# Kernel tuning notes

Hardware: AMD Instinct MI355X
Metric: run time of the kernel (lower is better)

The kernel has to match this reference:

```python
import jax, jax.numpy as jnp
import numpy as np

N, E, HID, H = 20000, 200000, 96, 6
HC = H * HID  # 576


def _ln(x, g, b):
    mu = x.mean(-1, keepdims=True)
    v = ((x - mu) ** 2).mean(-1, keepdims=True)
    return (x - mu) / jnp.sqrt(v + 1e-5) * g + b


def _gatv2(x, edge_emb, src, dst, Wl, bl, Wr, br, We, attw, cbias):
    # PyG GATv2Conv, concat=False, edge_dim=HID, eval mode (no dropout)
    xl = (x @ Wl + bl).reshape(N, H, HID)   # source transform (lin_l)
    xr = (x @ Wr + br).reshape(N, H, HID)   # target transform (lin_r)
    ee = (edge_emb @ We).reshape(E, H, HID) # lin_edge (no bias in PyG)
    h = jax.nn.leaky_relu(xl[src] + xr[dst] + ee, 0.2)   # [E,H,C]
    logits = jnp.einsum('ehc,hc->eh', h, attw)            # [E,H]
    m = jax.ops.segment_max(logits, dst, num_segments=N)  # segment softmax over dst
    ex = jnp.exp(logits - m[dst])
    den = jax.ops.segment_sum(ex, dst, num_segments=N)
    alpha = ex / (den[dst] + 1e-16)
    out = jax.ops.segment_sum(xl[src] * alpha[..., None], dst, num_segments=N)  # [N,H,C]
    return out.mean(axis=1) + cbias  # concat=False -> head mean, then bias


def _forward(x, edge_attr, ne_w, ne_b, ne_g, ne_beta, ee_w, ee_b, ee_g, ee_beta,
             Wl, bl, Wr, br, We, attw, cbias, lng, lnb,
             p1_w, p1_b, p1_g, p1_beta, p2_w, p2_b, p2_g, p2_beta, p3_w, p3_b,
             edge_index):
    src, dst = edge_index[0], edge_index[1]
    x = jax.nn.relu(_ln(x @ ne_w + ne_b, ne_g, ne_beta))
    edge_emb = jax.nn.relu(_ln(edge_attr @ ee_w + ee_b, ee_g, ee_beta))
    for i in range(3):  # fixed small layer count
        h = _gatv2(x, edge_emb, src, dst, Wl[i], bl[i], Wr[i], br[i], We[i], attw[i], cbias[i])
        if i < 2:
            h = jax.nn.elu(h)
        x = x + _ln(h, lng[i], lnb[i])
    ctx = jnp.concatenate([x[src], x[dst], edge_emb], axis=1)  # [E, 3*HID]
    h = jax.nn.relu(_ln(ctx @ p1_w + p1_b, p1_g, p1_beta))
    h = jax.nn.relu(_ln(h @ p2_w + p2_b, p2_g, p2_beta))
    return h @ p3_w + p3_b  # [E,1]


def setup_inputs():
    key = jax.random.key(0)
    ks = jax.random.split(key, 16)
    g = lambda k, shape, s: jax.random.normal(k, shape, dtype=jnp.float32) * s
    inp = {}
    inp['x'] = g(ks[0], (N, 4), 1.0)
    inp['edge_attr'] = g(ks[1], (E, 3), 1.0)
    inp['edge_index'] = jax.random.randint(ks[2], (2, E), 0, N, dtype=jnp.int32)
    # encoders
    inp['ne_w'] = g(ks[3], (4, HID), 0.5); inp['ne_b'] = jnp.zeros((HID,), jnp.float32)
    inp['ne_g'] = jnp.ones((HID,), jnp.float32); inp['ne_beta'] = jnp.zeros((HID,), jnp.float32)
    inp['ee_w'] = g(ks[4], (3, HID), 0.5); inp['ee_b'] = jnp.zeros((HID,), jnp.float32)
    inp['ee_g'] = jnp.ones((HID,), jnp.float32); inp['ee_beta'] = jnp.zeros((HID,), jnp.float32)
    # 3 stacked GATv2 layers
    inp['Wl'] = g(ks[5], (3, HID, HC), 0.1); inp['bl'] = jnp.zeros((3, HC), jnp.float32)
    inp['Wr'] = g(ks[6], (3, HID, HC), 0.1); inp['br'] = jnp.zeros((3, HC), jnp.float32)
    inp['We'] = g(ks[7], (3, HID, HC), 0.1)
    inp['attw'] = g(ks[8], (3, H, HID), 0.1)
    inp['cbias'] = jnp.zeros((3, HID), jnp.float32)
    inp['lng'] = jnp.ones((3, HID), jnp.float32); inp['lnb'] = jnp.zeros((3, HID), jnp.float32)
    # predictor MLP
    inp['p1_w'] = g(ks[9], (3 * HID, 128), 0.1); inp['p1_b'] = jnp.zeros((128,), jnp.float32)
    inp['p1_g'] = jnp.ones((128,), jnp.float32); inp['p1_beta'] = jnp.zeros((128,), jnp.float32)
    inp['p2_w'] = g(ks[10], (128, 64), 0.1); inp['p2_b'] = jnp.zeros((64,), jnp.float32)
    inp['p2_g'] = jnp.ones((64,), jnp.float32); inp['p2_beta'] = jnp.zeros((64,), jnp.float32)
    inp['p3_w'] = g(ks[11], (64, 1), 0.1); inp['p3_b'] = jnp.zeros((1,), jnp.float32)
    return inp


def reference(x, edge_attr, edge_index, ne_w, ne_b, ne_g, ne_beta, ee_w, ee_b, ee_g, ee_beta,
              Wl, bl, Wr, br, We, attw, cbias, lng, lnb,
              p1_w, p1_b, p1_g, p1_beta, p2_w, p2_b, p2_g, p2_beta, p3_w, p3_b):
    return _forward(x, edge_attr, ne_w, ne_b, ne_g, ne_beta, ee_w, ee_b, ee_g, ee_beta,
                    Wl, bl, Wr, br, We, attw, cbias, lng, lnb,
                    p1_w, p1_b, p1_g, p1_beta, p2_w, p2_b, p2_g, p2_beta, p3_w, p3_b,
                    edge_index)
```

## Files before the change

### kernel.cpp

```cpp
#include <hip/hip_runtime.h>
#include <math.h>

#define NN 20000
#define NE 200000

typedef __attribute__((ext_vector_type(8))) short bf16x8;
typedef __attribute__((ext_vector_type(8))) unsigned short u16x8;
typedef __attribute__((ext_vector_type(4))) float f32x4;

__device__ __forceinline__ unsigned short f2bf(float x) {
  union { float f; unsigned u; } c; c.f = x;
  unsigned r = c.u + 0x7FFF + ((c.u >> 16) & 1);
  return (unsigned short)(r >> 16);
}
__device__ __forceinline__ float bf2f(unsigned short u) {
  union { unsigned u; float f; } c; c.u = ((unsigned)u) << 16;
  return c.f;
}

template <int D>
__global__ __launch_bounds__(256) void encode_row_kernel(
    const float* __restrict__ in,
    const float* __restrict__ W, const float* __restrict__ b,
    const float* __restrict__ g, const float* __restrict__ beta,
    float* __restrict__ out, unsigned short* __restrict__ outb, int R) {
  int row = blockIdx.x * 256 + threadIdx.x;
  if (row >= R) return;
  float vin[D];
#pragma unroll
  for (int k = 0; k < D; k++) vin[k] = in[(size_t)row * D + k];
  float y[96];
  float s = 0.f, s2 = 0.f;
#pragma unroll
  for (int j = 0; j < 96; j++) {
    float v = b[j];
#pragma unroll
    for (int k = 0; k < D; k++) v += vin[k] * W[k * 96 + j];
    y[j] = v;
    s += v;
    s2 += v * v;
  }
  float mu = s * (1.f / 96.f);
  float var = s2 * (1.f / 96.f) - mu * mu;
  float rs = rsqrtf(var + 1e-5f);
#pragma unroll
  for (int c = 0; c < 12; c++) {
    u16x8 pk;
    float yo[8];
#pragma unroll
    for (int j = 0; j < 8; j++) {
      int jj = c * 8 + j;
      float v = (y[jj] - mu) * rs * g[jj] + beta[jj];
      v = fmaxf(v, 0.f);
      yo[j] = v;
      pk[j] = f2bf(v);
    }
    *(u16x8*)&outb[(size_t)row * 96 + c * 8] = pk;
    if (out) {
      f32x4 o0 = {yo[0], yo[1], yo[2], yo[3]};
      f32x4 o1 = {yo[4], yo[5], yo[6], yo[7]};
      *(f32x4*)&out[(size_t)row * 96 + c * 8] = o0;
      *(f32x4*)&out[(size_t)row * 96 + c * 8 + 4] = o1;
    }
  }
}

__global__ void convW_kernel(const float* __restrict__ We,
                             unsigned short* __restrict__ WeTb,
                             const float* __restrict__ Wl,
                             unsigned short* __restrict__ WlTb,
                             const float* __restrict__ Wr,
                             unsigned short* __restrict__ WrTb,
                             const float* __restrict__ p1w,
                             unsigned short* __restrict__ p1wT,
                             const float* __restrict__ p2w,
                             unsigned short* __restrict__ p2wT) {
  int idx = blockIdx.x * 256 + threadIdx.x;
  if (idx < 3 * 576 * 96) {
    int l = idx / (576 * 96);
    int rem = idx % (576 * 96);
    int n = rem / 96, k = rem % 96;
    size_t sidx = (size_t)l * 96 * 576 + (size_t)k * 576 + n;
    WeTb[idx] = f2bf(We[sidx]);
    WlTb[idx] = f2bf(Wl[sidx]);
    WrTb[idx] = f2bf(Wr[sidx]);
  }
  if (idx < 128 * 288) {
    int n = idx / 288, k = idx % 288;
    p1wT[idx] = f2bf(p1w[(size_t)k * 128 + n]);
  }
  if (idx < 64 * 128) {
    int n = idx / 128, k = idx % 128;
    p2wT[idx] = f2bf(p2w[(size_t)k * 64 + n]);
  }
}

__global__ void hist_kernel(const int* __restrict__ dst, int* __restrict__ deg) {
  int e = blockIdx.x * blockDim.x + threadIdx.x;
  if (e < NE) atomicAdd(&deg[dst[e]], 1);
}

__global__ __launch_bounds__(1024) void scan_kernel(
    const int* __restrict__ deg, int* __restrict__ rowptr, int* __restrict__ cursor) {
  __shared__ int wsum[16];
  int t = threadIdx.x;
  int base = t * 20;
  int loc[20];
  int s = 0;
#pragma unroll
  for (int j = 0; j < 20; j++) {
    int idx = base + j;
    int v = (idx < NN) ? deg[idx] : 0;
    loc[j] = s;
    s += v;
  }
  int lane = t & 63, wv = t >> 6;
  int inc = s;
#pragma unroll
  for (int off = 1; off < 64; off <<= 1) {
    int up = __shfl_up(inc, off);
    if (lane >= off) inc += up;
  }
  if (lane == 63) wsum[wv] = inc;
  __syncthreads();
  if (wv == 0) {
    int wval = (lane < 16) ? wsum[lane] : 0;
#pragma unroll
    for (int off = 1; off < 16; off <<= 1) {
      int up = __shfl_up(wval, off);
      if (lane >= off) wval += up;
    }
    if (lane < 16) wsum[lane] = wval;
  }
  __syncthreads();
  int wbase = (wv > 0) ? wsum[wv - 1] : 0;
  int excl = wbase + inc - s;
#pragma unroll
  for (int j = 0; j < 20; j++) {
    int idx = base + j;
    if (idx < NN) { rowptr[idx] = excl + loc[j]; cursor[idx] = excl + loc[j]; }
  }
  if (t == 0) rowptr[NN] = NE;
}

__global__ void scatter_kernel(const int* __restrict__ src,
                               const int* __restrict__ dst,
                               int* __restrict__ cursor, int* __restrict__ eidx,
                               int* __restrict__ srcp, int* __restrict__ dstp) {
  int e = blockIdx.x * blockDim.x + threadIdx.x;
  if (e < NE) {
    int d = dst[e];
    int p = atomicAdd(&cursor[d], 1);
    eidx[p] = e;
    srcp[p] = src[e];
    dstp[p] = d;
  }
}

__global__ __launch_bounds__(256) void xlxr_mfma_kernel(
    const unsigned short* __restrict__ Xb,
    const unsigned short* __restrict__ WlTb,
    const float* __restrict__ bl,
    const unsigned short* __restrict__ WrTb,
    const float* __restrict__ br,
    unsigned short* __restrict__ xlb, unsigned short* __restrict__ xrb) {
  int t = threadIdx.x;
  int wave = t >> 6, lane = t & 63;
  int l15 = lane & 15, quad = lane >> 4;
  int node = blockIdx.x * 64 + wave * 16 + l15;
  int nclamp = (node < NN) ? node : (NN - 1);
  bool valid = node < NN;
  const unsigned short* brow = &Xb[(size_t)nclamp * 96 + quad * 8];
  bf16x8 b0 = *(const bf16x8*)&brow[0];
  bf16x8 b1 = *(const bf16x8*)&brow[32];
  bf16x8 b2 = *(const bf16x8*)&brow[64];
#pragma unroll
  for (int mt = 0; mt < 36; mt++) {
    int wc = mt * 16 + l15;
    const unsigned short* aL = &WlTb[(size_t)wc * 96 + quad * 8];
    f32x4 accL = {0.f, 0.f, 0.f, 0.f};
    accL = __builtin_amdgcn_mfma_f32_16x16x32_bf16(*(const bf16x8*)&aL[0], b0, accL, 0, 0, 0);
    accL = __builtin_amdgcn_mfma_f32_16x16x32_bf16(*(const bf16x8*)&aL[32], b1, accL, 0, 0, 0);
    accL = __builtin_amdgcn_mfma_f32_16x16x32_bf16(*(const bf16x8*)&aL[64], b2, accL, 0, 0, 0);
    const unsigned short* aR = &WrTb[(size_t)wc * 96 + quad * 8];
    f32x4 accR = {0.f, 0.f, 0.f, 0.f};
    accR = __builtin_amdgcn_mfma_f32_16x16x32_bf16(*(const bf16x8*)&aR[0], b0, accR, 0, 0, 0);
    accR = __builtin_amdgcn_mfma_f32_16x16x32_bf16(*(const bf16x8*)&aR[32], b1, accR, 0, 0, 0);
    accR = __builtin_amdgcn_mfma_f32_16x16x32_bf16(*(const bf16x8*)&aR[64], b2, accR, 0, 0, 0);
    if (valid) {
      int c0 = mt * 16 + quad * 4;
      float4 bbL = *(const float4*)&bl[c0];
      float4 bbR = *(const float4*)&br[c0];
      ushort4 pL, pR;
      pL.x = f2bf(accL[0] + bbL.x); pL.y = f2bf(accL[1] + bbL.y);
      pL.z = f2bf(accL[2] + bbL.z); pL.w = f2bf(accL[3] + bbL.w);
      pR.x = f2bf(accR[0] + bbR.x); pR.y = f2bf(accR[1] + bbR.y);
      pR.z = f2bf(accR[2] + bbR.z); pR.w = f2bf(accR[3] + bbR.w);
      *(ushort4*)&xlb[(size_t)node * 576 + c0] = pL;
      *(ushort4*)&xrb[(size_t)node * 576 + c0] = pR;
    }
  }
}

__global__ __launch_bounds__(256) void logits_mfma_kernel(
    const unsigned short* __restrict__ EMBb,
    const unsigned short* __restrict__ WeTb,
    const float* __restrict__ attw,
    const unsigned short* __restrict__ XLb,
    const unsigned short* __restrict__ XRb,
    const int* __restrict__ eidx, const int* __restrict__ srcp,
    const int* __restrict__ dstp,
    float* __restrict__ logp) {
  __shared__ __align__(16) unsigned short emb[64][104];
  __shared__ __align__(16) unsigned short eeb[64][200];
  __shared__ int sd[64][2];
  int t = threadIdx.x;
  int p0 = blockIdx.x * 64;
  if (t < 128) sd[t >> 1][t & 1] = (t & 1) ? dstp[p0 + (t >> 1)] : srcp[p0 + (t >> 1)];
  {
    int e = t >> 2, c0 = (t & 3) * 24;
    int erow = eidx[p0 + e];
    const unsigned short* sp = &EMBb[(size_t)erow * 96 + c0];
    *(bf16x8*)&emb[e][c0]      = *(const bf16x8*)&sp[0];
    *(bf16x8*)&emb[e][c0 + 8]  = *(const bf16x8*)&sp[8];
    *(bf16x8*)&emb[e][c0 + 16] = *(const bf16x8*)&sp[16];
  }
  __syncthreads();

  int wave = t >> 6, lane = t & 63;
  int l15 = lane & 15, quad = lane >> 4;
  int el = t >> 2;
  int cq = (t & 3) * 24;
  int gsrc = sd[el][0];
  int gdst = sd[el][1];

  for (int hp = 0; hp < 3; hp++) {
    int h0 = hp * 2, h1 = hp * 2 + 1;
    const unsigned short* xl0 = &XLb[(size_t)gsrc * 576 + h0 * 96 + cq];
    const unsigned short* xr0 = &XRb[(size_t)gdst * 576 + h0 * 96 + cq];
    const unsigned short* xl1 = &XLb[(size_t)gsrc * 576 + h1 * 96 + cq];
    const unsigned short* xr1 = &XRb[(size_t)gdst * 576 + h1 * 96 + cq];
    bf16x8 gl0[3], gr0[3], gl1[3], gr1[3];
#pragma unroll
    for (int c8 = 0; c8 < 3; c8++) {
      gl0[c8] = *(const bf16x8*)&xl0[c8 * 8];
      gr0[c8] = *(const bf16x8*)&xr0[c8 * 8];
      gl1[c8] = *(const bf16x8*)&xl1[c8 * 8];
      gr1[c8] = *(const bf16x8*)&xr1[c8 * 8];
    }
#pragma unroll
    for (int k = 0; k < 3; k++) {
      int ntg = wave * 3 + k;
      int col = hp * 192 + ntg * 16 + l15;
      const unsigned short* brow = &WeTb[(size_t)col * 96 + quad * 8];
      bf16x8 b0 = *(const bf16x8*)&brow[0];
      bf16x8 b1 = *(const bf16x8*)&brow[32];
      bf16x8 b2 = *(const bf16x8*)&brow[64];
#pragma unroll
      for (int et = 0; et < 4; et++) {
        const unsigned short* ar = &emb[et * 16 + l15][quad * 8];
        bf16x8 a0 = *(const bf16x8*)&ar[0];
        bf16x8 a1 = *(const bf16x8*)&ar[32];
        bf16x8 a2 = *(const bf16x8*)&ar[64];
        f32x4 acc = {0.f, 0.f, 0.f, 0.f};
        acc = __builtin_amdgcn_mfma_f32_16x16x32_bf16(a0, b0, acc, 0, 0, 0);
        acc = __builtin_amdgcn_mfma_f32_16x16x32_bf16(a1, b1, acc, 0, 0, 0);
        acc = __builtin_amdgcn_mfma_f32_16x16x32_bf16(a2, b2, acc, 0, 0, 0);
#pragma unroll
        for (int r = 0; r < 4; r++)
          eeb[et * 16 + quad * 4 + r][ntg * 16 + l15] = f2bf(acc[r]);
      }
    }
    __syncthreads();
    float pl0 = 0.f, pl1 = 0.f;
    {
      const unsigned short* ee0 = &eeb[el][cq];
      const unsigned short* ee1 = &eeb[el][96 + cq];
      const f32x4* ap0 = (const f32x4*)&attw[h0 * 96 + cq];
      const f32x4* ap1 = (const f32x4*)&attw[h1 * 96 + cq];
#pragma unroll
      for (int c8 = 0; c8 < 3; c8++) {
        bf16x8 ev0 = *(const bf16x8*)&ee0[c8 * 8];
        bf16x8 ev1 = *(const bf16x8*)&ee1[c8 * 8];
        f32x4 a00 = ap0[c8 * 2], a01 = ap0[c8 * 2 + 1];
        f32x4 a10 = ap1[c8 * 2], a11 = ap1[c8 * 2 + 1];
#pragma unroll
        for (int j = 0; j < 4; j++) {
          float v0 = bf2f((unsigned short)ev0[j]) +
                     bf2f((unsigned short)gl0[c8][j]) +
                     bf2f((unsigned short)gr0[c8][j]);
          v0 = (v0 > 0.f) ? v0 : 0.2f * v0;
          pl0 += v0 * a00[j];
          float w0 = bf2f((unsigned short)ev0[j + 4]) +
                     bf2f((unsigned short)gl0[c8][j + 4]) +
                     bf2f((unsigned short)gr0[c8][j + 4]);
          w0 = (w0 > 0.f) ? w0 : 0.2f * w0;
          pl0 += w0 * a01[j];
          float v1 = bf2f((unsigned short)ev1[j]) +
                     bf2f((unsigned short)gl1[c8][j]) +
                     bf2f((unsigned short)gr1[c8][j]);
          v1 = (v1 > 0.f) ? v1 : 0.2f * v1;
          pl1 += v1 * a10[j];
          float w1 = bf2f((unsigned short)ev1[j + 4]) +
                     bf2f((unsigned short)gl1[c8][j + 4]) +
                     bf2f((unsigned short)gr1[c8][j + 4]);
          w1 = (w1 > 0.f) ? w1 : 0.2f * w1;
          pl1 += w1 * a11[j];
        }
      }
    }
    pl0 += __shfl_xor(pl0, 1); pl0 += __shfl_xor(pl0, 2);
    pl1 += __shfl_xor(pl1, 1); pl1 += __shfl_xor(pl1, 2);
    if ((t & 3) == 0) {
      size_t base = (size_t)(p0 + el) * 6 + hp * 2;
      logp[base] = pl0;
      logp[base + 1] = pl1;
    }
    __syncthreads();
  }
}

__global__ __launch_bounds__(256) void alpha_kernel(
    const float* __restrict__ logp, const int* __restrict__ rowptr,
    float* __restrict__ alpha) {
  int node = blockIdx.x * 4 + (threadIdx.x >> 6);
  int lane = threadIdx.x & 63;
  if (node >= NN) return;
  int r0 = rowptr[node], r1 = rowptr[node + 1];
  int d = r1 - r0;
  if (d == 0) return;
  if (d <= 64) {
    bool act = lane < d;
    int p = r0 + (act ? lane : (d - 1));
    float lg[6];
#pragma unroll
    for (int h = 0; h < 6; h++) lg[h] = logp[(size_t)p * 6 + h];
#pragma unroll
    for (int h = 0; h < 6; h++) {
      float m = act ? lg[h] : -1e30f;
#pragma unroll
      for (int off = 32; off > 0; off >>= 1) m = fmaxf(m, __shfl_xor(m, off));
      float w = act ? expf(lg[h] - m) : 0.f;
      float s = w;
#pragma unroll
      for (int off = 32; off > 0; off >>= 1) s += __shfl_xor(s, off);
      if (act) alpha[(size_t)p * 6 + h] = w / (s + 1e-16f);
    }
  } else {
    float m[6], s[6];
#pragma unroll
    for (int h = 0; h < 6; h++) { m[h] = -1e30f; s[h] = 0.f; }
    for (int cs = 0; cs < d; cs += 64) {
      int cnt = min(64, d - cs);
      bool act = lane < cnt;
      int p = r0 + cs + (act ? lane : (cnt - 1));
#pragma unroll
      for (int h = 0; h < 6; h++) {
        float lg = act ? logp[(size_t)p * 6 + h] : -1e30f;
        float cm = lg;
#pragma unroll
        for (int off = 32; off > 0; off >>= 1) cm = fmaxf(cm, __shfl_xor(cm, off));
        float newm = fmaxf(m[h], cm);
        float w = act ? expf(lg - newm) : 0.f;
        float ss = w;
#pragma unroll
        for (int off = 32; off > 0; off >>= 1) ss += __shfl_xor(ss, off);
        s[h] = s[h] * expf(m[h] - newm) + ss;
        m[h] = newm;
      }
    }
    float inv[6];
#pragma unroll
    for (int h = 0; h < 6; h++) inv[h] = 1.f / (s[h] + 1e-16f);
    for (int cs = 0; cs < d; cs += 64) {
      int cnt = min(64, d - cs);
      if (lane < cnt) {
        int p = r0 + cs + lane;
#pragma unroll
        for (int h = 0; h < 6; h++)
          alpha[(size_t)p * 6 + h] =
              expf(logp[(size_t)p * 6 + h] - m[h]) * inv[h];
      }
    }
  }
}

__global__ __launch_bounds__(576) void aggregate_kernel(
    float* __restrict__ x, unsigned short* __restrict__ xb,
    const unsigned short* __restrict__ XLb,
    const float* __restrict__ alpha, const int* __restrict__ rowptr,
    const int* __restrict__ srcp,
    const float* __restrict__ cbias, const float* __restrict__ lng,
    const float* __restrict__ lnb, int do_elu) {
  int t = threadIdx.x;
  int nb = t / 96, c = t % 96;
  int n = blockIdx.x * 6 + nb;
  bool vn = (n < NN);
  __shared__ float fin[6][96];
  __shared__ float red[6][2];
  int wave = t >> 6, lane = t & 63;
  int r0 = 0, d = 0;
  if (vn) { r0 = rowptr[n]; d = rowptr[n + 1] - r0; }
  float acc = 0.f;
  int j = 0;
  for (; j + 1 < d; j += 2) {
    int p = r0 + j;
    int s0 = srcp[p], s1 = srcp[p + 1];
    const float* ap0 = &alpha[(size_t)p * 6];
    float2 a00 = *(const float2*)&ap0[0];
    float2 a01 = *(const float2*)&ap0[2];
    float2 a02 = *(const float2*)&ap0[4];
    float2 a10 = *(const float2*)&ap0[6];
    float2 a11 = *(const float2*)&ap0[8];
    float2 a12 = *(const float2*)&ap0[10];
    const unsigned short* xp0 = &XLb[(size_t)s0 * 576 + c];
    const unsigned short* xp1 = &XLb[(size_t)s1 * 576 + c];
    unsigned short v00 = xp0[0],   v01 = xp0[96],  v02 = xp0[192];
    unsigned short v03 = xp0[288], v04 = xp0[384], v05 = xp0[480];
    unsigned short v10 = xp1[0],   v11 = xp1[96],  v12 = xp1[192];
    unsigned short v13 = xp1[288], v14 = xp1[384], v15 = xp1[480];
    acc += a00.x * bf2f(v00) + a00.y * bf2f(v01) + a01.x * bf2f(v02) +
           a01.y * bf2f(v03) + a02.x * bf2f(v04) + a02.y * bf2f(v05);
    acc += a10.x * bf2f(v10) + a10.y * bf2f(v11) + a11.x * bf2f(v12) +
           a11.y * bf2f(v13) + a12.x * bf2f(v14) + a12.y * bf2f(v15);
  }
  if (j < d) {
    int p = r0 + j;
    int s0 = srcp[p];
    const float* ap0 = &alpha[(size_t)p * 6];
    float2 a00 = *(const float2*)&ap0[0];
    float2 a01 = *(const float2*)&ap0[2];
    float2 a02 = *(const float2*)&ap0[4];
    const unsigned short* xp0 = &XLb[(size_t)s0 * 576 + c];
    unsigned short v00 = xp0[0],   v01 = xp0[96],  v02 = xp0[192];
    unsigned short v03 = xp0[288], v04 = xp0[384], v05 = xp0[480];
    acc += a00.x * bf2f(v00) + a00.y * bf2f(v01) + a01.x * bf2f(v02) +
           a01.y * bf2f(v03) + a02.x * bf2f(v04) + a02.y * bf2f(v05);
  }
  float fv = 0.f;
  if (vn) {
    float s = acc * (1.f / 6.f) + cbias[c];
    if (do_elu) s = (s > 0.f) ? s : expm1f(s);
    fv = s;
  }
  fin[nb][c] = fv;
  __syncthreads();
  if (wave < 6) {
    float x0 = fin[wave][lane];
    float x1 = (lane < 32) ? fin[wave][64 + lane] : 0.f;
    float s = x0 + x1;
    float s2 = x0 * x0 + x1 * x1;
#pragma unroll
    for (int off = 32; off > 0; off >>= 1) {
      s += __shfl_xor(s, off);
      s2 += __shfl_xor(s2, off);
    }
    if (lane == 0) {
      float mu = s * (1.f / 96.f);
      float var = s2 * (1.f / 96.f) - mu * mu;
      red[wave][0] = mu;
      red[wave][1] = rsqrtf(var + 1e-5f);
    }
  }
  __syncthreads();
  if (vn) {
    float y = (fv - red[nb][0]) * red[nb][1] * lng[c] + lnb[c];
    float nv = x[(size_t)n * 96 + c] + y;
    x[(size_t)n * 96 + c] = nv;
    xb[(size_t)n * 96 + c] = f2bf(nv);
  }
}

__global__ __launch_bounds__(256) void pred_mfma_kernel(
    const unsigned short* __restrict__ Xb,
    const unsigned short* __restrict__ EMBb,
    const int* __restrict__ src, const int* __restrict__ dst,
    const unsigned short* __restrict__ p1wT,
    const float* __restrict__ p1b, const float* __restrict__ p1g,
    const float* __restrict__ p1be,
    const unsigned short* __restrict__ p2wT,
    const float* __restrict__ p2b, const float* __restrict__ p2g,
    const float* __restrict__ p2be,
    const float* __restrict__ p3w, const float* __restrict__ p3b,
    float* __restrict__ out) {
  __shared__ __align__(16) unsigned short fragB[4 * 9 * 64 * 8];
  __shared__ unsigned short h1s[4][16][136];
  int t = threadIdx.x;
  int wave = t >> 6, lane = t & 63;
  int l15 = lane & 15, quad = lane >> 4;
  int ebase = blockIdx.x * 64 + wave * 16;
  int erow = ebase + l15;
  int sN = src[erow], dN = dst[erow];

  bf16x8 A[9];
  const unsigned short* xs = &Xb[(size_t)sN * 96 + quad * 8];
  const unsigned short* xd = &Xb[(size_t)dN * 96 + quad * 8];
  const unsigned short* em = &EMBb[(size_t)erow * 96 + quad * 8];
#pragma unroll
  for (int c = 0; c < 3; c++) {
    A[c]     = *(const bf16x8*)&xs[c * 32];
    A[c + 3] = *(const bf16x8*)&xd[c * 32];
    A[c + 6] = *(const bf16x8*)&em[c * 32];
  }

  {
    bf16x8 tmp[9];
#pragma unroll
    for (int c = 0; c < 9; c++)
      tmp[c] = *(const bf16x8*)&p1wT[(size_t)(wave * 16 + l15) * 288 + c * 32 + quad * 8];
#pragma unroll
    for (int c = 0; c < 9; c++)
      *(bf16x8*)&fragB[((wave * 9 + c) * 64 + lane) * 8] = tmp[c];
  }
  __syncthreads();

  f32x4 C1[8];
#pragma unroll
  for (int nt = 0; nt < 4; nt++) {
    f32x4 acc = {0.f, 0.f, 0.f, 0.f};
#pragma unroll
    for (int c = 0; c < 9; c++) {
      bf16x8 B = *(const bf16x8*)&fragB[((nt * 9 + c) * 64 + lane) * 8];
      acc = __builtin_amdgcn_mfma_f32_16x16x32_bf16(A[c], B, acc, 0, 0, 0);
    }
    float bias = p1b[nt * 16 + l15];
    acc[0] += bias; acc[1] += bias; acc[2] += bias; acc[3] += bias;
    C1[nt] = acc;
  }
  __syncthreads();
  {
    bf16x8 tmp[9];
#pragma unroll
    for (int c = 0; c < 9; c++)
      tmp[c] = *(const bf16x8*)&p1wT[(size_t)((4 + wave) * 16 + l15) * 288 + c * 32 + quad * 8];
#pragma unroll
    for (int c = 0; c < 9; c++)
      *(bf16x8*)&fragB[((wave * 9 + c) * 64 + lane) * 8] = tmp[c];
  }
  __syncthreads();
#pragma unroll
  for (int nt = 4; nt < 8; nt++) {
    f32x4 acc = {0.f, 0.f, 0.f, 0.f};
#pragma unroll
    for (int c = 0; c < 9; c++) {
      bf16x8 B = *(const bf16x8*)&fragB[(((nt - 4) * 9 + c) * 64 + lane) * 8];
      acc = __builtin_amdgcn_mfma_f32_16x16x32_bf16(A[c], B, acc, 0, 0, 0);
    }
    float bias = p1b[nt * 16 + l15];
    acc[0] += bias; acc[1] += bias; acc[2] += bias; acc[3] += bias;
    C1[nt] = acc;
  }
  __syncthreads();
  {
    bf16x8 tmp[4];
#pragma unroll
    for (int c = 0; c < 4; c++)
      tmp[c] = *(const bf16x8*)&p2wT[(size_t)(wave * 16 + l15) * 128 + c * 32 + quad * 8];
#pragma unroll
    for (int c = 0; c < 4; c++)
      *(bf16x8*)&fragB[((wave * 4 + c) * 64 + lane) * 8] = tmp[c];
  }

  float mu1[4], rs1[4];
#pragma unroll
  for (int r = 0; r < 4; r++) {
    float s = 0.f, s2 = 0.f;
#pragma unroll
    for (int nt = 0; nt < 8; nt++) { float v = C1[nt][r]; s += v; s2 += v * v; }
    s += __shfl_xor(s, 1);  s += __shfl_xor(s, 2);
    s += __shfl_xor(s, 4);  s += __shfl_xor(s, 8);
    s2 += __shfl_xor(s2, 1); s2 += __shfl_xor(s2, 2);
    s2 += __shfl_xor(s2, 4); s2 += __shfl_xor(s2, 8);
    float mu = s * (1.f / 128.f);
    float var = s2 * (1.f / 128.f) - mu * mu;
    mu1[r] = mu;
    rs1[r] = rsqrtf(var + 1e-5f);
  }
#pragma unroll
  for (int nt = 0; nt < 8; nt++) {
    float g = p1g[nt * 16 + l15], be = p1be[nt * 16 + l15];
#pragma unroll
    for (int r = 0; r < 4; r++) {
      float v = (C1[nt][r] - mu1[r]) * rs1[r] * g + be;
      v = fmaxf(v, 0.f);
      h1s[wave][quad * 4 + r][nt * 16 + l15] = f2bf(v);
    }
  }
  __syncthreads();

  f32x4 C2[4];
#pragma unroll
  for (int nt = 0; nt < 4; nt++) {
    f32x4 acc = {0.f, 0.f, 0.f, 0.f};
#pragma unroll
    for (int c = 0; c < 4; c++) {
      bf16x8 Af = *(const bf16x8*)&h1s[wave][l15][c * 32 + quad * 8];
      bf16x8 B = *(const bf16x8*)&fragB[((nt * 4 + c) * 64 + lane) * 8];
      acc = __builtin_amdgcn_mfma_f32_16x16x32_bf16(Af, B, acc, 0, 0, 0);
    }
    float bias = p2b[nt * 16 + l15];
    acc[0] += bias; acc[1] += bias; acc[2] += bias; acc[3] += bias;
    C2[nt] = acc;
  }

  float mu2[4], rs2[4];
#pragma unroll
  for (int r = 0; r < 4; r++) {
    float s = 0.f, s2 = 0.f;
#pragma unroll
    for (int nt = 0; nt < 4; nt++) { float v = C2[nt][r]; s += v; s2 += v * v; }
    s += __shfl_xor(s, 1);  s += __shfl_xor(s, 2);
    s += __shfl_xor(s, 4);  s += __shfl_xor(s, 8);
    s2 += __shfl_xor(s2, 1); s2 += __shfl_xor(s2, 2);
    s2 += __shfl_xor(s2, 4); s2 += __shfl_xor(s2, 8);
    float mu = s * (1.f / 64.f);
    float var = s2 * (1.f / 64.f) - mu * mu;
    mu2[r] = mu;
    rs2[r] = rsqrtf(var + 1e-5f);
  }

  float partial[4] = {0.f, 0.f, 0.f, 0.f};
#pragma unroll
  for (int nt = 0; nt < 4; nt++) {
    float g = p2g[nt * 16 + l15], be = p2be[nt * 16 + l15];
    float pw = p3w[nt * 16 + l15];
#pragma unroll
    for (int r = 0; r < 4; r++) {
      float v = (C2[nt][r] - mu2[r]) * rs2[r] * g + be;
      v = fmaxf(v, 0.f);
      partial[r] += v * pw;
    }
  }
#pragma unroll
  for (int r = 0; r < 4; r++) {
    float p = partial[r];
    p += __shfl_xor(p, 1);
    p += __shfl_xor(p, 2);
    p += __shfl_xor(p, 4);
    p += __shfl_xor(p, 8);
    partial[r] = p;
  }
  if (l15 == 0) {
    float b3 = p3b[0];
#pragma unroll
    for (int r = 0; r < 4; r++)
      out[ebase + quad * 4 + r] = partial[r] + b3;
  }
}

static inline size_t alignup(size_t v) { return (v + 255) & ~(size_t)255; }

extern "C" void kernel_launch(void* const* d_in, const int* in_sizes, int n_in,
                              void* d_out, int out_size, void* d_ws, size_t ws_size,
                              hipStream_t stream) {
  const float* x_in      = (const float*)d_in[0];
  const float* edge_attr = (const float*)d_in[1];
  const int*   ei        = (const int*)d_in[2];
  const int* src = ei;
  const int* dst = ei + NE;
  const float* ne_w = (const float*)d_in[3];
  const float* ne_b = (const float*)d_in[4];
  const float* ne_g = (const float*)d_in[5];
  const float* ne_be = (const float*)d_in[6];
  const float* ee_w = (const float*)d_in[7];
  const float* ee_b = (const float*)d_in[8];
  const float* ee_g = (const float*)d_in[9];
  const float* ee_be = (const float*)d_in[10];
  const float* Wl = (const float*)d_in[11];
  const float* bl = (const float*)d_in[12];
  const float* Wr = (const float*)d_in[13];
  const float* br = (const float*)d_in[14];
  const float* We = (const float*)d_in[15];
  const float* attw = (const float*)d_in[16];
  const float* cbias = (const float*)d_in[17];
  const float* lng = (const float*)d_in[18];
  const float* lnb = (const float*)d_in[19];
  const float* p1w = (const float*)d_in[20];
  const float* p1b = (const float*)d_in[21];
  const float* p1g = (const float*)d_in[22];
  const float* p1be = (const float*)d_in[23];
  const float* p2w = (const float*)d_in[24];
  const float* p2b = (const float*)d_in[25];
  const float* p2g = (const float*)d_in[26];
  const float* p2be = (const float*)d_in[27];
  const float* p3w = (const float*)d_in[28];
  const float* p3b = (const float*)d_in[29];
  float* out = (float*)d_out;

  char* w = (char*)d_ws;
  float* X    = (float*)w; w += alignup((size_t)NN * 96 * 4);
  float* LOG  = (float*)w; w += alignup((size_t)NE * 6 * 4);
  float* ALPHA = (float*)w; w += alignup((size_t)NE * 6 * 4);
  unsigned short* EMBb = (unsigned short*)w; w += alignup((size_t)NE * 96 * 2);
  unsigned short* XLb  = (unsigned short*)w; w += alignup((size_t)NN * 576 * 2);
  unsigned short* XRb  = (unsigned short*)w; w += alignup((size_t)NN * 576 * 2);
  unsigned short* Xb   = (unsigned short*)w; w += alignup((size_t)NN * 96 * 2);
  unsigned short* WeTb = (unsigned short*)w; w += alignup((size_t)3 * 576 * 96 * 2);
  unsigned short* WlTb = (unsigned short*)w; w += alignup((size_t)3 * 576 * 96 * 2);
  unsigned short* WrTb = (unsigned short*)w; w += alignup((size_t)3 * 576 * 96 * 2);
  unsigned short* p1wT = (unsigned short*)w; w += alignup((size_t)128 * 288 * 2);
  unsigned short* p2wT = (unsigned short*)w; w += alignup((size_t)64 * 128 * 2);
  int* deg    = (int*)w; w += alignup((size_t)(NN + 1) * 4);
  int* rowptr = (int*)w; w += alignup((size_t)(NN + 1) * 4);
  int* cursor = (int*)w; w += alignup((size_t)NN * 4);
  int* eidx   = (int*)w; w += alignup((size_t)NE * 4);
  int* srcp   = (int*)w; w += alignup((size_t)NE * 4);
  int* dstp   = (int*)w; w += alignup((size_t)NE * 4);

  encode_row_kernel<4><<<(NN + 255) / 256, 256, 0, stream>>>(
      x_in, ne_w, ne_b, ne_g, ne_be, X, Xb, NN);
  encode_row_kernel<3><<<(NE + 255) / 256, 256, 0, stream>>>(
      edge_attr, ee_w, ee_b, ee_g, ee_be, nullptr, EMBb, NE);
  convW_kernel<<<(3 * 576 * 96 + 255) / 256, 256, 0, stream>>>(
      We, WeTb, Wl, WlTb, Wr, WrTb, p1w, p1wT, p2w, p2wT);

  hipMemsetAsync(deg, 0, (size_t)(NN + 1) * 4, stream);
  hist_kernel<<<(NE + 255) / 256, 256, 0, stream>>>(dst, deg);
  scan_kernel<<<1, 1024, 0, stream>>>(deg, rowptr, cursor);
  scatter_kernel<<<(NE + 255) / 256, 256, 0, stream>>>(src, dst, cursor, eidx,
                                                       srcp, dstp);

  for (int i = 0; i < 3; i++) {
    const unsigned short* WlT_i = WlTb + (size_t)i * 576 * 96;
    const float* bl_i = bl + (size_t)i * 576;
    const unsigned short* WrT_i = WrTb + (size_t)i * 576 * 96;
    const float* br_i = br + (size_t)i * 576;
    const unsigned short* WeT_i = WeTb + (size_t)i * 576 * 96;
    const float* aw_i = attw + (size_t)i * 576;
    const float* cb_i = cbias + (size_t)i * 96;
    const float* lg_i = lng + (size_t)i * 96;
    const float* lb_i = lnb + (size_t)i * 96;
    xlxr_mfma_kernel<<<(NN + 63) / 64, 256, 0, stream>>>(Xb, WlT_i, bl_i,
                                                         WrT_i, br_i, XLb, XRb);
    logits_mfma_kernel<<<NE / 64, 256, 0, stream>>>(EMBb, WeT_i, aw_i, XLb, XRb,
                                                    eidx, srcp, dstp, LOG);
    alpha_kernel<<<(NN + 3) / 4, 256, 0, stream>>>(LOG, rowptr, ALPHA);
    aggregate_kernel<<<(NN + 5) / 6, 576, 0, stream>>>(X, Xb, XLb, ALPHA,
                                                       rowptr, srcp,
                                                       cb_i, lg_i, lb_i,
                                                       (i < 2) ? 1 : 0);
  }

  pred_mfma_kernel<<<NE / 64, 256, 0, stream>>>(Xb, EMBb, src, dst,
                                                p1wT, p1b, p1g, p1be,
                                                p2wT, p2b, p2g, p2be,
                                                p3w, p3b, out);
}
```

Baseline: 864.6 us.

## Transpose logits MFMA so edge-embedding products stay in registers, staging We in LDS

The logits kernel now computes We^T·emb with edges on the MFMA N dimension, so each wave owns 16 edges and consumes the accumulator fragments directly for the leaky-relu and attention dot product. This removes the bf16 round-trip of the edge-embedding product through the shared eeb buffer, along with its barrier and its extra rounding. The We slice for each head pair is cooperatively staged into padded LDS instead of being read per wave from global memory. In exchange it adds two barriers per head pair for restaging, and XL/XR gathers become 8-byte loads spread across lanes rather than 16-byte contiguous chunks.

```diff
diff --git a/kernel.cpp b/kernel.cpp
--- a/kernel.cpp
+++ b/kernel.cpp
@@ -212,7 +212,7 @@
     const int* __restrict__ dstp,
     float* __restrict__ logp) {
   __shared__ __align__(16) unsigned short emb[64][104];
-  __shared__ __align__(16) unsigned short eeb[64][200];
+  __shared__ __align__(16) unsigned short WeL[192 * 100];
   __shared__ int sd[64][2];
   int t = threadIdx.x;
   int p0 = blockIdx.x * 64;
@@ -225,98 +225,79 @@
     *(bf16x8*)&emb[e][c0 + 8]  = *(const bf16x8*)&sp[8];
     *(bf16x8*)&emb[e][c0 + 16] = *(const bf16x8*)&sp[16];
   }
+  {
+#pragma unroll
+    for (int i = 0; i < 9; i++) {
+      int c = t + i * 256;
+      int row = c / 12, off = (c % 12) * 8;
+      bf16x8 v = *(const bf16x8*)&WeTb[(size_t)row * 96 + off];
+      *(bf16x8*)&WeL[row * 100 + off] = v;
+    }
+  }
   __syncthreads();
 
   int wave = t >> 6, lane = t & 63;
   int l15 = lane & 15, quad = lane >> 4;
-  int el = t >> 2;
-  int cq = (t & 3) * 24;
-  int gsrc = sd[el][0];
-  int gdst = sd[el][1];
+  int edge = wave * 16 + l15;
+  int gsrc = sd[edge][0];
+  int gdst = sd[edge][1];
+  bf16x8 B0 = *(const bf16x8*)&emb[edge][quad * 8];
+  bf16x8 B1 = *(const bf16x8*)&emb[edge][32 + quad * 8];
+  bf16x8 B2 = *(const bf16x8*)&emb[edge][64 + quad * 8];
 
   for (int hp = 0; hp < 3; hp++) {
-    int h0 = hp * 2, h1 = hp * 2 + 1;
-    const unsigned short* xl0 = &XLb[(size_t)gsrc * 576 + h0 * 96 + cq];
-    const unsigned short* xr0 = &XRb[(size_t)gdst * 576 + h0 * 96 + cq];
-    const unsigned short* xl1 = &XLb[(size_t)gsrc * 576 + h1 * 96 + cq];
-    const unsigned short* xr1 = &XRb[(size_t)gdst * 576 + h1 * 96 + cq];
-    bf16x8 gl0[3], gr0[3], gl1[3], gr1[3];
-#pragma unroll
-    for (int c8 = 0; c8 < 3; c8++) {
-      gl0[c8] = *(const bf16x8*)&xl0[c8 * 8];
-      gr0[c8] = *(const bf16x8*)&xr0[c8 * 8];
-      gl1[c8] = *(const bf16x8*)&xl1[c8 * 8];
-      gr1[c8] = *(const bf16x8*)&xr1[c8 * 8];
-    }
-#pragma unroll
-    for (int k = 0; k < 3; k++) {
-      int ntg = wave * 3 + k;
-      int col = hp * 192 + ntg * 16 + l15;
-      const unsigned short* brow = &WeTb[(size_t)col * 96 + quad * 8];
-      bf16x8 b0 = *(const bf16x8*)&brow[0];
-      bf16x8 b1 = *(const bf16x8*)&brow[32];
-      bf16x8 b2 = *(const bf16x8*)&brow[64];
-#pragma unroll
-      for (int et = 0; et < 4; et++) {
-        const unsigned short* ar = &emb[et * 16 + l15][quad * 8];
-        bf16x8 a0 = *(const bf16x8*)&ar[0];
-        bf16x8 a1 = *(const bf16x8*)&ar[32];
-        bf16x8 a2 = *(const bf16x8*)&ar[64];
+    if (hp > 0) {
+      __syncthreads();
+#pragma unroll
+      for (int i = 0; i < 9; i++) {
+        int c = t + i * 256;
+        int row = c / 12, off = (c % 12) * 8;
+        bf16x8 v = *(const bf16x8*)&WeTb[(size_t)(hp * 192 + row) * 96 + off];
+        *(bf16x8*)&WeL[row * 100 + off] = v;
+      }
+      __syncthreads();
+    }
+#pragma unroll
+    for (int half = 0; half < 2; half++) {
+      ushort4 gl[6], gr[6];
+#pragma unroll
+      for (int i = 0; i < 6; i++) {
+        int gcol = hp * 192 + (half * 6 + i) * 16 + quad * 4;
+        gl[i] = *(const ushort4*)&XLb[(size_t)gsrc * 576 + gcol];
+        gr[i] = *(const ushort4*)&XRb[(size_t)gdst * 576 + gcol];
+      }
+      float p = 0.f;
+#pragma unroll
+      for (int i = 0; i < 6; i++) {
+        int nt = half * 6 + i;
+        const unsigned short* ap = &WeL[(nt * 16 + l15) * 100];
         f32x4 acc = {0.f, 0.f, 0.f, 0.f};
-        acc = __builtin_amdgcn_mfma_f32_16x16x32_bf16(a0, b0, acc, 0, 0, 0);
-        acc = __builtin_amdgcn_mfma_f32_16x16x32_bf16(a1, b1, acc, 0, 0, 0);
-        acc = __builtin_amdgcn_mfma_f32_16x16x32_bf16(a2, b2, acc, 0, 0, 0);
-#pragma unroll
-        for (int r = 0; r < 4; r++)
-          eeb[et * 16 + quad * 4 + r][ntg * 16 + l15] = f2bf(acc[r]);
+        acc = __builtin_amdgcn_mfma_f32_16x16x32_bf16(
+            *(const bf16x8*)&ap[quad * 8], B0, acc, 0, 0, 0);
+        acc = __builtin_amdgcn_mfma_f32_16x16x32_bf16(
+            *(const bf16x8*)&ap[32 + quad * 8], B1, acc, 0, 0, 0);
+        acc = __builtin_amdgcn_mfma_f32_16x16x32_bf16(
+            *(const bf16x8*)&ap[64 + quad * 8], B2, acc, 0, 0, 0);
+        int gcol = hp * 192 + nt * 16 + quad * 4;
+        float4 aw = *(const float4*)&attw[gcol];
+        float v0 = acc[0] + bf2f(gl[i].x) + bf2f(gr[i].x);
+        v0 = (v0 > 0.f) ? v0 : 0.2f * v0;
+        p += v0 * aw.x;
+        float v1 = acc[1] + bf2f(gl[i].y) + bf2f(gr[i].y);
+        v1 = (v1 > 0.f) ? v1 : 0.2f * v1;
+        p += v1 * aw.y;
+        float v2 = acc[2] + bf2f(gl[i].z) + bf2f(gr[i].z);
+        v2 = (v2 > 0.f) ? v2 : 0.2f * v2;
+        p += v2 * aw.z;
+        float v3 = acc[3] + bf2f(gl[i].w) + bf2f(gr[i].w);
+        v3 = (v3 > 0.f) ? v3 : 0.2f * v3;
+        p += v3 * aw.w;
       }
-    }
-    __syncthreads();
-    float pl0 = 0.f, pl1 = 0.f;
-    {
-      const unsigned short* ee0 = &eeb[el][cq];
-      const unsigned short* ee1 = &eeb[el][96 + cq];
-      const f32x4* ap0 = (const f32x4*)&attw[h0 * 96 + cq];
-      const f32x4* ap1 = (const f32x4*)&attw[h1 * 96 + cq];
-#pragma unroll
-      for (int c8 = 0; c8 < 3; c8++) {
-        bf16x8 ev0 = *(const bf16x8*)&ee0[c8 * 8];
-        bf16x8 ev1 = *(const bf16x8*)&ee1[c8 * 8];
-        f32x4 a00 = ap0[c8 * 2], a01 = ap0[c8 * 2 + 1];
-        f32x4 a10 = ap1[c8 * 2], a11 = ap1[c8 * 2 + 1];
-#pragma unroll
-        for (int j = 0; j < 4; j++) {
-          float v0 = bf2f((unsigned short)ev0[j]) +
-                     bf2f((unsigned short)gl0[c8][j]) +
-                     bf2f((unsigned short)gr0[c8][j]);
-          v0 = (v0 > 0.f) ? v0 : 0.2f * v0;
-          pl0 += v0 * a00[j];
-          float w0 = bf2f((unsigned short)ev0[j + 4]) +
-                     bf2f((unsigned short)gl0[c8][j + 4]) +
-                     bf2f((unsigned short)gr0[c8][j + 4]);
-          w0 = (w0 > 0.f) ? w0 : 0.2f * w0;
-          pl0 += w0 * a01[j];
-          float v1 = bf2f((unsigned short)ev1[j]) +
-                     bf2f((unsigned short)gl1[c8][j]) +
-                     bf2f((unsigned short)gr1[c8][j]);
-          v1 = (v1 > 0.f) ? v1 : 0.2f * v1;
-          pl1 += v1 * a10[j];
-          float w1 = bf2f((unsigned short)ev1[j + 4]) +
-                     bf2f((unsigned short)gl1[c8][j + 4]) +
-                     bf2f((unsigned short)gr1[c8][j + 4]);
-          w1 = (w1 > 0.f) ? w1 : 0.2f * w1;
-          pl1 += w1 * a11[j];
-        }
-      }
-    }
-    pl0 += __shfl_xor(pl0, 1); pl0 += __shfl_xor(pl0, 2);
-    pl1 += __shfl_xor(pl1, 1); pl1 += __shfl_xor(pl1, 2);
-    if ((t & 3) == 0) {
-      size_t base = (size_t)(p0 + el) * 6 + hp * 2;
-      logp[base] = pl0;
-      logp[base + 1] = pl1;
-    }
-    __syncthreads();
+      p += __shfl_xor(p, 16);
+      p += __shfl_xor(p, 32);
+      if (quad == 0)
+        logp[(size_t)(p0 + edge) * 6 + hp * 2 + half] = p;
+    }
   }
 }
 
```

Result: slower. 1.131 ms (+30.8%).
